# Optimization experiments

Hardware: AMD Instinct MI355X
Metric: run time of the kernel (lower is better)

## Reference

```python
import jax, jax.numpy as jnp
import numpy as np

NUM_USERS = 50000
NUM_ITEMS = 40000
EMB = 64
NNZ = 2_000_000
BATCH = 1024


def setup_inputs() -> dict:
    key = jax.random.key(0)
    ks = jax.random.split(key, 10)
    graph_rows = jax.random.randint(ks[0], (NNZ,), 0, NUM_USERS, dtype=jnp.int32)
    graph_cols = jax.random.randint(ks[1], (NNZ,), 0, NUM_ITEMS, dtype=jnp.int32)
    graph_vals = jax.random.uniform(ks[2], (NNZ,), dtype=jnp.float32)
    Wq = jax.random.normal(ks[3], (2 * EMB, NUM_ITEMS), dtype=jnp.float32) * 0.01
    bq = jnp.zeros((2 * EMB,), jnp.float32)
    Wp = jax.random.normal(ks[4], (NUM_ITEMS, EMB), dtype=jnp.float32) * 0.01
    bp = jnp.zeros((NUM_ITEMS,), jnp.float32)
    user = jax.random.randint(ks[5], (BATCH,), 0, NUM_USERS, dtype=jnp.int32)
    x = (jax.random.uniform(ks[6], (BATCH, NUM_ITEMS)) < 0.02).astype(jnp.float32)
    eps = jax.random.normal(ks[7], (NUM_USERS, EMB), dtype=jnp.float32)
    return dict(graph_vals=graph_vals, Wq=Wq, bq=bq, Wp=Wp, bp=bp, x=x,
                eps=eps, graph_rows=graph_rows, graph_cols=graph_cols, user=user)


def reference(graph_vals, Wq, bq, Wp, bp, x, eps, graph_rows, graph_cols, user):
    # ---- encode: single SpMM  h = Graph @ Wq^T + bq   (dropout off / eval mode)
    # gather item rows of Wq^T per nonzero, scale, scatter-add into users
    gathered = graph_vals[:, None] * Wq.T[graph_cols]          # [nnz, 2E]
    h = jax.ops.segment_sum(gathered, graph_rows, num_segments=NUM_USERS) + bq  # [U, 2E]
    mu, logvar = h[:, :EMB], h[:, EMB:]                        # [U, E] each
    # ---- reparameterize: z = mu + eps * exp(0.5*logvar)
    z = mu + eps * jnp.exp(0.5 * logvar)
    # ---- decode batch users: single Linear(E -> I)
    zb = z[user]                                               # [B, E]
    recon = zb @ Wp.T + bp                                     # [B, I]
    # ---- Mult-VAE ELBO (anneal = 1.0)
    log_sm = jax.nn.log_softmax(recon, axis=-1)
    recon_loss = -jnp.mean(jnp.sum(log_sm * x, axis=-1))
    mu_b, lv_b = mu[user], logvar[user]
    kl_loss = -0.5 * jnp.mean(jnp.sum(1.0 + lv_b - mu_b * mu_b - jnp.exp(lv_b), axis=-1))
    return jnp.stack([recon_loss, kl_loss])  # [2]: (recon_loss, KL_loss)
```

## Files before the change

kernel.cpp:

```cpp
#include <hip/hip_runtime.h>
#include <cstdint>

#define NUM_USERS 50000
#define NUM_ITEMS 40000
#define EMB 64
#define NNZ_E 2000000
#define BATCH 1024
#define NCHB 125
#define SLOT_CAP 128
#define INF_I 0x7fffffff
#define SC_BLK 7813

typedef __attribute__((ext_vector_type(8))) short short8;
typedef __attribute__((ext_vector_type(4))) float float4v;

__device__ __forceinline__ unsigned short f2bf(float f) {
    union { float f; unsigned u; } x; x.f = f;
    unsigned r = x.u + 0x7fffu + ((x.u >> 16) & 1u);
    return (unsigned short)(r >> 16);
}
__device__ __forceinline__ float bf2f(unsigned short s) {
    return __uint_as_float(((unsigned)s) << 16);
}
__device__ __forceinline__ unsigned pack01(float lo, float hi) {
    return __builtin_amdgcn_perm(__float_as_uint(hi), __float_as_uint(lo), 0x07060302u);
}

__global__ __launch_bounds__(256) void k_init(int* __restrict__ map, int* __restrict__ cnt,
                                              float* __restrict__ scal, int2* __restrict__ compact) {
    int t = blockIdx.x * blockDim.x + threadIdx.x;
    if (t < NUM_USERS) map[t] = INF_I;
    if (t < BATCH) cnt[t] = 0;
    if (t < 4) scal[t] = 0.f;
    if (t < BATCH * SLOT_CAP) compact[t] = make_int2(0, 0);
}

__global__ void k_map(const int* __restrict__ user, int* __restrict__ map) {
    int i = blockIdx.x * blockDim.x + threadIdx.x;
    if (i < BATCH) atomicMin(&map[user[i]], i);
}

__global__ __launch_bounds__(256) void k_prepsc(const int* __restrict__ rows,
                                                const int* __restrict__ cols,
                                                const float* __restrict__ vals,
                                                const int* __restrict__ map,
                                                int* __restrict__ cnt,
                                                int2* __restrict__ compact,
                                                const float* __restrict__ Wq,
                                                const float* __restrict__ Wp,
                                                const float* __restrict__ bp,
                                                unsigned short* __restrict__ WqT,
                                                unsigned short* __restrict__ WpBf,
                                                unsigned short* __restrict__ WpT,
                                                unsigned short* __restrict__ bpBf) {
    __shared__ float t2f[160 * 65];
    const int bid = blockIdx.x;
    const int tid = threadIdx.x;
    if (bid < SC_BLK) {
        const int e = bid * 256 + tid;
        if (e >= NNZ_E) return;
        int s = map[rows[e]];
        if (s == INF_I) return;
        int pos = atomicAdd(&cnt[s], 1);
        if (pos < SLOT_CAP) compact[s * SLOT_CAP + pos] = make_int2(cols[e], __float_as_int(vals[e]));
        return;
    }
    const int pb = bid - SC_BLK;
    if (pb < 1250) {
        const int jb = pb * 32;
        for (int idx = tid; idx < 4096; idx += 256) {
            int d = idx >> 5, c = idx & 31;
            t2f[d * 33 + c] = Wq[(size_t)d * NUM_ITEMS + jb + c];
        }
        __syncthreads();
        for (int idx = tid; idx < 4096; idx += 256) {
            int j = idx >> 7, d = idx & 127;
            WqT[(size_t)(jb + j) * 128 + d] = f2bf(t2f[d * 33 + j]);
        }
    } else if (pb < 3750) {
        const int e0 = ((pb - 1250) * 256 + tid) * 4;
        float4 w = *(const float4*)&Wp[e0];
        ushort4 o;
        o.x = f2bf(w.x); o.y = f2bf(w.y); o.z = f2bf(w.z); o.w = f2bf(w.w);
        *(ushort4*)&WpBf[e0] = o;
    } else if (pb < 4000) {
        const int j0 = (pb - 3750) * 160;
        for (int idx = tid; idx < 10240; idx += 256) {
            int jl = idx >> 6, d = idx & 63;
            t2f[jl * 65 + d] = Wp[(size_t)(j0 + jl) * 64 + d];
        }
        __syncthreads();
        for (int idx = tid; idx < 10240; idx += 256) {
            int d = idx / 160, jl = idx - d * 160;
            WpT[(size_t)d * NUM_ITEMS + j0 + jl] = f2bf(t2f[jl * 65 + d]);
        }
    } else {
        const int e0 = ((pb - 4000) * 256 + tid) * 4;
        if (e0 < NUM_ITEMS) {
            float4 w = *(const float4*)&bp[e0];
            ushort4 o;
            o.x = f2bf(w.x); o.y = f2bf(w.y); o.z = f2bf(w.z); o.w = f2bf(w.w);
            *(ushort4*)&bpBf[e0] = o;
        }
    }
}

__global__ __launch_bounds__(256) void k_hz(const int* __restrict__ user,
                                            const int* __restrict__ map,
                                            const int* __restrict__ cnt,
                                            const int2* __restrict__ compact,
                                            const unsigned short* __restrict__ WqT,
                                            const float* __restrict__ bq,
                                            const float* __restrict__ eps,
                                            unsigned short* __restrict__ zbBf,
                                            float* __restrict__ zF32,
                                            float* __restrict__ scal) {
    __shared__ float sh[4][128];
    const int i = blockIdx.x;
    const int tid = threadIdx.x;
    const int w = tid >> 6, lane = tid & 63;
    const int u = user[i];
    const int s = map[u];
    const int n8 = (min(cnt[s], SLOT_CAP) + 7) & ~7;
    const int2* cp = compact + s * SLOT_CAP;
    float ax = 0.f, ay = 0.f;
    for (int e = w; e < n8; e += 8) {
        int2 c0 = cp[e], c1 = cp[e + 4];
        ushort2 w0 = *(const ushort2*)&WqT[(size_t)c0.x * 128 + lane * 2];
        ushort2 w1 = *(const ushort2*)&WqT[(size_t)c1.x * 128 + lane * 2];
        float v0 = __int_as_float(c0.y), v1 = __int_as_float(c1.y);
        ax = fmaf(v0, bf2f(w0.x), ax);
        ay = fmaf(v0, bf2f(w0.y), ay);
        ax = fmaf(v1, bf2f(w1.x), ax);
        ay = fmaf(v1, bf2f(w1.y), ay);
    }
    sh[w][lane * 2] = ax;
    sh[w][lane * 2 + 1] = ay;
    __syncthreads();
    float h = 0.f;
    if (tid < 128) h = sh[0][tid] + sh[1][tid] + sh[2][tid] + sh[3][tid] + bq[tid];
    __syncthreads();
    if (tid < 128) sh[0][tid] = h;
    __syncthreads();
    if (tid < 64) {
        float mu = sh[0][tid];
        float lv = sh[0][tid + 64];
        float z = fmaf(eps[(size_t)u * EMB + tid], __expf(0.5f * lv), mu);
        zbBf[i * EMB + tid] = f2bf(z);
        zF32[i * EMB + tid] = z;
        float kl = 1.0f + lv - mu * mu - __expf(lv);
        #pragma unroll
        for (int o = 32; o; o >>= 1) kl += __shfl_down(kl, o);
        if (tid == 0) atomicAdd(&scal[1], kl);
    }
}

__global__ __launch_bounds__(256) void k_xz(const float* __restrict__ x,
                                            const unsigned short* __restrict__ WpT,
                                            const unsigned short* __restrict__ bpBf,
                                            const float* __restrict__ zF32,
                                            const unsigned short* __restrict__ zbBf,
                                            const unsigned short* __restrict__ WpBf,
                                            const float* __restrict__ bp,
                                            float4* __restrict__ part4) {
    const int tid = threadIdx.x;
    const int wid = tid >> 6, lane = tid & 63;
    const int l15 = lane & 15, quad = lane >> 4;
    const int kc = blockIdx.x;
    const int ibase = blockIdx.y * 128 + wid * 32;

    float4v acc[2][4], accA[2];
    #pragma unroll
    for (int mt = 0; mt < 2; mt++) {
        accA[mt] = (float4v){0.f, 0.f, 0.f, 0.f};
        #pragma unroll
        for (int nt = 0; nt < 4; nt++) acc[mt][nt] = (float4v){0.f, 0.f, 0.f, 0.f};
    }
    #pragma unroll
    for (int st = 0; st < 10; st++) {
        const int kb = kc * 320 + st * 32;
        short8 af[2];
        #pragma unroll
        for (int mt = 0; mt < 2; mt++) {
            const float* px = x + (size_t)(ibase + mt * 16 + l15) * NUM_ITEMS + kb + quad * 8;
            float4 a0 = *(const float4*)px;
            float4 a1 = *(const float4*)(px + 4);
            union { short8 s; unsigned u[4]; } v;
            v.u[0] = pack01(a0.x, a0.y);
            v.u[1] = pack01(a0.z, a0.w);
            v.u[2] = pack01(a1.x, a1.y);
            v.u[3] = pack01(a1.z, a1.w);
            af[mt] = v.s;
        }
        short8 bfr[4];
        #pragma unroll
        for (int nt = 0; nt < 4; nt++)
            bfr[nt] = *(const short8*)&WpT[(size_t)(nt * 16 + l15) * NUM_ITEMS + kb + quad * 8];
        short8 ab;
        if (l15 == 0) {
            ab = *(const short8*)&bpBf[kb + quad * 8];
        } else if (l15 == 1) {
            short o = (short)0x3F80;
            ab = (short8){o, o, o, o, o, o, o, o};
        } else {
            ab = (short8){0, 0, 0, 0, 0, 0, 0, 0};
        }
        #pragma unroll
        for (int mt = 0; mt < 2; mt++) {
            #pragma unroll
            for (int nt = 0; nt < 4; nt++)
                acc[mt][nt] = __builtin_amdgcn_mfma_f32_16x16x32_bf16(
                    af[mt], bfr[nt], acc[mt][nt], 0, 0, 0);
            accA[mt] = __builtin_amdgcn_mfma_f32_16x16x32_bf16(
                    af[mt], ab, accA[mt], 0, 0, 0);
        }
    }
    float c_s[2][4], sx_s[2][4];
    #pragma unroll
    for (int mt = 0; mt < 2; mt++) {
        #pragma unroll
        for (int r = 0; r < 4; r++) {
            const int row = ibase + mt * 16 + quad * 4 + r;
            float dxp = 0.f;
            #pragma unroll
            for (int nt = 0; nt < 4; nt++)
                dxp += zF32[(size_t)row * EMB + nt * 16 + l15] * acc[mt][nt][r];
            #pragma unroll
            for (int d = 1; d < 16; d <<= 1) dxp += __shfl_xor(dxp, d);
            sx_s[mt][r] = __shfl(accA[mt][r], (lane & 48) + 1);
            c_s[mt][r] = dxp + accA[mt][r];
        }
    }

    short8 zf[2][2];
    #pragma unroll
    for (int mt = 0; mt < 2; mt++) {
        const unsigned short* pa = zbBf + (size_t)(ibase + mt * 16 + l15) * EMB + quad * 8;
        zf[mt][0] = *(const short8*)pa;
        zf[mt][1] = *(const short8*)(pa + 32);
    }
    float m_run[2][4], s_run[2][4];
    #pragma unroll
    for (int mt = 0; mt < 2; mt++)
        #pragma unroll
        for (int r = 0; r < 4; r++) { m_run[mt][r] = -1e30f; s_run[mt][r] = 0.f; }

    #pragma unroll
    for (int c5 = 0; c5 < 5; c5++) {
        const int jb = kc * 320 + c5 * 64;
        short8 bfr2[4][2];
        #pragma unroll
        for (int nt = 0; nt < 4; nt++) {
            const unsigned short* pb = WpBf + (size_t)(jb + nt * 16 + l15) * EMB + quad * 8;
            bfr2[nt][0] = *(const short8*)pb;
            bfr2[nt][1] = *(const short8*)(pb + 32);
        }
        float4v accz[2][4];
        #pragma unroll
        for (int mt = 0; mt < 2; mt++)
            #pragma unroll
            for (int nt = 0; nt < 4; nt++)
                accz[mt][nt] = (float4v){0.f, 0.f, 0.f, 0.f};
        #pragma unroll
        for (int kh = 0; kh < 2; kh++)
            #pragma unroll
            for (int mt = 0; mt < 2; mt++)
                #pragma unroll
                for (int nt = 0; nt < 4; nt++)
                    accz[mt][nt] = __builtin_amdgcn_mfma_f32_16x16x32_bf16(
                        zf[mt][kh], bfr2[nt][kh], accz[mt][nt], 0, 0, 0);
        float bpv[4];
        #pragma unroll
        for (int nt = 0; nt < 4; nt++) bpv[nt] = bp[jb + nt * 16 + l15];
        #pragma unroll
        for (int mt = 0; mt < 2; mt++) {
            #pragma unroll
            for (int r = 0; r < 4; r++) {
                float v0 = accz[mt][0][r] + bpv[0];
                float v1 = accz[mt][1][r] + bpv[1];
                float v2 = accz[mt][2][r] + bpv[2];
                float v3 = accz[mt][3][r] + bpv[3];
                float mx = fmaxf(fmaxf(v0, v1), fmaxf(v2, v3));
                float M2 = fmaxf(m_run[mt][r], mx);
                float ls = __expf(v0 - M2) + __expf(v1 - M2) +
                           __expf(v2 - M2) + __expf(v3 - M2);
                s_run[mt][r] = s_run[mt][r] * __expf(m_run[mt][r] - M2) + ls;
                m_run[mt][r] = M2;
            }
        }
    }
    #pragma unroll
    for (int d = 1; d < 16; d <<= 1) {
        #pragma unroll
        for (int mt = 0; mt < 2; mt++)
            #pragma unroll
            for (int r = 0; r < 4; r++) {
                float m2 = __shfl_xor(m_run[mt][r], d);
                float s2 = __shfl_xor(s_run[mt][r], d);
                float M = fmaxf(m_run[mt][r], m2);
                s_run[mt][r] = s_run[mt][r] * __expf(m_run[mt][r] - M)
                             + s2 * __expf(m2 - M);
                m_run[mt][r] = M;
            }
    }
    if (l15 == 0) {
        #pragma unroll
        for (int mt = 0; mt < 2; mt++)
            #pragma unroll
            for (int r = 0; r < 4; r++) {
                const int row = ibase + mt * 16 + quad * 4 + r;
                part4[(size_t)row * NCHB + kc] =
                    make_float4(m_run[mt][r], s_run[mt][r], c_s[mt][r], sx_s[mt][r]);
            }
    }
}

__global__ __launch_bounds__(64) void k_merge(const float4* __restrict__ part4,
                                              float* __restrict__ scal,
                                              float* __restrict__ out) {
    const int row = blockIdx.x;
    const int lane = threadIdx.x;
    float M = -1e30f, S = 0.f, dxc = 0.f, sx = 0.f;
    for (int c = lane; c < NCHB; c += 64) {
        float4 p = part4[(size_t)row * NCHB + c];
        float M2 = fmaxf(M, p.x);
        S = S * __expf(M - M2) + p.y * __expf(p.x - M2);
        M = M2; dxc += p.z; sx += p.w;
    }
    #pragma unroll
    for (int o = 1; o < 64; o <<= 1) {
        float M2 = __shfl_xor(M, o);
        float S2 = __shfl_xor(S, o);
        float Mn = fmaxf(M, M2);
        S = S * __expf(M - Mn) + S2 * __expf(M2 - Mn);
        M = Mn;
        dxc += __shfl_xor(dxc, o);
        sx += __shfl_xor(sx, o);
    }
    if (lane == 0) {
        float lse = M + logf(S);
        atomicAdd(&scal[0], dxc - lse * sx);
        __threadfence();
        unsigned done = atomicAdd((unsigned*)&scal[2], 1u);
        if (done == BATCH - 1) {
            float recon = atomicAdd(&scal[0], 0.f);
            float kl = atomicAdd(&scal[1], 0.f);
            out[0] = -recon * (1.0f / BATCH);
            out[1] = -0.5f * kl * (1.0f / BATCH);
        }
    }
}

extern "C" void kernel_launch(void* const* d_in, const int* in_sizes, int n_in,
                              void* d_out, int out_size, void* d_ws, size_t ws_size,
                              hipStream_t stream) {
    const float* graph_vals = (const float*)d_in[0];
    const float* Wq         = (const float*)d_in[1];
    const float* bq         = (const float*)d_in[2];
    const float* Wp         = (const float*)d_in[3];
    const float* bp         = (const float*)d_in[4];
    const float* x          = (const float*)d_in[5];
    const float* eps        = (const float*)d_in[6];
    const int*   graph_rows = (const int*)d_in[7];
    const int*   graph_cols = (const int*)d_in[8];
    const int*   user       = (const int*)d_in[9];
    float* out = (float*)d_out;

    char* ws = (char*)d_ws;
    int*            map     = (int*)(ws + 0);
    int*            cnt     = (int*)(ws + 200704);
    float*          scal    = (float*)(ws + 204800);
    int2*           compact = (int2*)(ws + 205056);
    unsigned short* zbBf    = (unsigned short*)(ws + 1253632);
    float*          zF32    = (float*)(ws + 1384704);
    float4*         part4   = (float4*)(ws + 1646848);
    unsigned short* WpBf    = (unsigned short*)(ws + 3694848);
    unsigned short* WqT     = (unsigned short*)(ws + 8814848);
    unsigned short* WpT     = (unsigned short*)(ws + 19054848);
    unsigned short* bpBf    = (unsigned short*)(ws + 24174848);

    k_init<<<512, 256, 0, stream>>>(map, cnt, scal, compact);
    k_map<<<4, 256, 0, stream>>>(user, map);
    k_prepsc<<<SC_BLK + 4040, 256, 0, stream>>>(graph_rows, graph_cols, graph_vals, map, cnt,
                                                compact, Wq, Wp, bp, WqT, WpBf, WpT, bpBf);
    k_hz<<<BATCH, 256, 0, stream>>>(user, map, cnt, compact, WqT, bq, eps, zbBf, zF32, scal);
    dim3 g(NCHB, BATCH / 128);
    k_xz<<<g, 256, 0, stream>>>(x, WpT, bpBf, zF32, zbBf, WpBf, bp, part4);
    k_merge<<<BATCH, 64, 0, stream>>>(part4, scal, out);
}
```

Before: 388.9 us.

## Split scatter and weight prep kernels; use one-wave blocks for xz

```diff
diff --git a/kernel.cpp b/kernel.cpp
--- a/kernel.cpp
+++ b/kernel.cpp
@@ -9,7 +9,6 @@
 #define NCHB 125
 #define SLOT_CAP 128
 #define INF_I 0x7fffffff
-#define SC_BLK 7813
 
 typedef __attribute__((ext_vector_type(8))) short short8;
 typedef __attribute__((ext_vector_type(4))) float float4v;
@@ -40,34 +39,32 @@
     if (i < BATCH) atomicMin(&map[user[i]], i);
 }
 
-__global__ __launch_bounds__(256) void k_prepsc(const int* __restrict__ rows,
-                                                const int* __restrict__ cols,
-                                                const float* __restrict__ vals,
-                                                const int* __restrict__ map,
-                                                int* __restrict__ cnt,
-                                                int2* __restrict__ compact,
-                                                const float* __restrict__ Wq,
-                                                const float* __restrict__ Wp,
-                                                const float* __restrict__ bp,
-                                                unsigned short* __restrict__ WqT,
-                                                unsigned short* __restrict__ WpBf,
-                                                unsigned short* __restrict__ WpT,
-                                                unsigned short* __restrict__ bpBf) {
-    __shared__ float t2f[160 * 65];
+__global__ __launch_bounds__(256) void k_scatter(const int* __restrict__ rows,
+                                                 const int* __restrict__ cols,
+                                                 const float* __restrict__ vals,
+                                                 const int* __restrict__ map,
+                                                 int* __restrict__ cnt,
+                                                 int2* __restrict__ compact) {
+    const int e = blockIdx.x * 256 + threadIdx.x;
+    if (e >= NNZ_E) return;
+    int s = map[rows[e]];
+    if (s == INF_I) return;
+    int pos = atomicAdd(&cnt[s], 1);
+    if (pos < SLOT_CAP) compact[s * SLOT_CAP + pos] = make_int2(cols[e], __float_as_int(vals[e]));
+}
+
+__global__ __launch_bounds__(256) void k_prep(const float* __restrict__ Wq,
+                                              const float* __restrict__ Wp,
+                                              const float* __restrict__ bp,
+                                              unsigned short* __restrict__ WqT,
+                                              unsigned short* __restrict__ WpBf,
+                                              unsigned short* __restrict__ WpT,
+                                              unsigned short* __restrict__ bpBf) {
+    __shared__ float t2f[4224];
     const int bid = blockIdx.x;
     const int tid = threadIdx.x;
-    if (bid < SC_BLK) {
-        const int e = bid * 256 + tid;
-        if (e >= NNZ_E) return;
-        int s = map[rows[e]];
-        if (s == INF_I) return;
-        int pos = atomicAdd(&cnt[s], 1);
-        if (pos < SLOT_CAP) compact[s * SLOT_CAP + pos] = make_int2(cols[e], __float_as_int(vals[e]));
-        return;
-    }
-    const int pb = bid - SC_BLK;
-    if (pb < 1250) {
-        const int jb = pb * 32;
+    if (bid < 1250) {
+        const int jb = bid * 32;
         for (int idx = tid; idx < 4096; idx += 256) {
             int d = idx >> 5, c = idx & 31;
             t2f[d * 33 + c] = Wq[(size_t)d * NUM_ITEMS + jb + c];
@@ -77,25 +74,25 @@
             int j = idx >> 7, d = idx & 127;
             WqT[(size_t)(jb + j) * 128 + d] = f2bf(t2f[d * 33 + j]);
         }
-    } else if (pb < 3750) {
-        const int e0 = ((pb - 1250) * 256 + tid) * 4;
+    } else if (bid < 3750) {
+        const int e0 = ((bid - 1250) * 256 + tid) * 4;
         float4 w = *(const float4*)&Wp[e0];
         ushort4 o;
         o.x = f2bf(w.x); o.y = f2bf(w.y); o.z = f2bf(w.z); o.w = f2bf(w.w);
         *(ushort4*)&WpBf[e0] = o;
-    } else if (pb < 4000) {
-        const int j0 = (pb - 3750) * 160;
-        for (int idx = tid; idx < 10240; idx += 256) {
+    } else if (bid < 4375) {
+        const int j0 = (bid - 3750) * 64;
+        for (int idx = tid; idx < 4096; idx += 256) {
             int jl = idx >> 6, d = idx & 63;
             t2f[jl * 65 + d] = Wp[(size_t)(j0 + jl) * 64 + d];
         }
         __syncthreads();
-        for (int idx = tid; idx < 10240; idx += 256) {
-            int d = idx / 160, jl = idx - d * 160;
+        for (int idx = tid; idx < 4096; idx += 256) {
+            int d = idx >> 6, jl = idx & 63;
             WpT[(size_t)d * NUM_ITEMS + j0 + jl] = f2bf(t2f[jl * 65 + d]);
         }
     } else {
-        const int e0 = ((pb - 4000) * 256 + tid) * 4;
+        const int e0 = ((bid - 4375) * 256 + tid) * 4;
         if (e0 < NUM_ITEMS) {
             float4 w = *(const float4*)&bp[e0];
             ushort4 o;
@@ -155,19 +152,18 @@
     }
 }
 
-__global__ __launch_bounds__(256) void k_xz(const float* __restrict__ x,
-                                            const unsigned short* __restrict__ WpT,
-                                            const unsigned short* __restrict__ bpBf,
-                                            const float* __restrict__ zF32,
-                                            const unsigned short* __restrict__ zbBf,
-                                            const unsigned short* __restrict__ WpBf,
-                                            const float* __restrict__ bp,
-                                            float4* __restrict__ part4) {
-    const int tid = threadIdx.x;
-    const int wid = tid >> 6, lane = tid & 63;
+__global__ __launch_bounds__(64) void k_xz(const float* __restrict__ x,
+                                           const unsigned short* __restrict__ WpT,
+                                           const unsigned short* __restrict__ bpBf,
+                                           const float* __restrict__ zF32,
+                                           const unsigned short* __restrict__ zbBf,
+                                           const unsigned short* __restrict__ WpBf,
+                                           const float* __restrict__ bp,
+                                           float4* __restrict__ part4) {
+    const int lane = threadIdx.x;
     const int l15 = lane & 15, quad = lane >> 4;
     const int kc = blockIdx.x;
-    const int ibase = blockIdx.y * 128 + wid * 32;
+    const int ibase = blockIdx.y * 32;
 
     float4v acc[2][4], accA[2];
     #pragma unroll
@@ -381,10 +377,10 @@
 
     k_init<<<512, 256, 0, stream>>>(map, cnt, scal, compact);
     k_map<<<4, 256, 0, stream>>>(user, map);
-    k_prepsc<<<SC_BLK + 4040, 256, 0, stream>>>(graph_rows, graph_cols, graph_vals, map, cnt,
-                                                compact, Wq, Wp, bp, WqT, WpBf, WpT, bpBf);
+    k_scatter<<<7813, 256, 0, stream>>>(graph_rows, graph_cols, graph_vals, map, cnt, compact);
+    k_prep<<<4415, 256, 0, stream>>>(Wq, Wp, bp, WqT, WpBf, WpT, bpBf);
     k_hz<<<BATCH, 256, 0, stream>>>(user, map, cnt, compact, WqT, bq, eps, zbBf, zF32, scal);
-    dim3 g(NCHB, BATCH / 128);
-    k_xz<<<g, 256, 0, stream>>>(x, WpT, bpBf, zF32, zbBf, WpBf, bp, part4);
+    dim3 g(NCHB, 32);
+    k_xz<<<g, 64, 0, stream>>>(x, WpT, bpBf, zF32, zbBf, WpBf, bp, part4);
     k_merge<<<BATCH, 64, 0, stream>>>(part4, scal, out);
 }
```

Result: no change. 390.6 us (+0.4%).

## Stage Wp tiles in LDS and software-pipeline x loads in k_xz

Applied to the files above, without the earlier changes.

```diff
diff --git a/kernel.cpp b/kernel.cpp
--- a/kernel.cpp
+++ b/kernel.cpp
@@ -53,7 +53,7 @@
                                                 unsigned short* __restrict__ WpBf,
                                                 unsigned short* __restrict__ WpT,
                                                 unsigned short* __restrict__ bpBf) {
-    __shared__ float t2f[160 * 65];
+    __shared__ float t2f[4224];
     const int bid = blockIdx.x;
     const int tid = threadIdx.x;
     if (bid < SC_BLK) {
@@ -83,19 +83,19 @@
         ushort4 o;
         o.x = f2bf(w.x); o.y = f2bf(w.y); o.z = f2bf(w.z); o.w = f2bf(w.w);
         *(ushort4*)&WpBf[e0] = o;
-    } else if (pb < 4000) {
-        const int j0 = (pb - 3750) * 160;
-        for (int idx = tid; idx < 10240; idx += 256) {
+    } else if (pb < 4375) {
+        const int j0 = (pb - 3750) * 64;
+        for (int idx = tid; idx < 4096; idx += 256) {
             int jl = idx >> 6, d = idx & 63;
             t2f[jl * 65 + d] = Wp[(size_t)(j0 + jl) * 64 + d];
         }
         __syncthreads();
-        for (int idx = tid; idx < 10240; idx += 256) {
-            int d = idx / 160, jl = idx - d * 160;
+        for (int idx = tid; idx < 4096; idx += 256) {
+            int d = idx >> 6, jl = idx & 63;
             WpT[(size_t)d * NUM_ITEMS + j0 + jl] = f2bf(t2f[jl * 65 + d]);
         }
     } else {
-        const int e0 = ((pb - 4000) * 256 + tid) * 4;
+        const int e0 = ((pb - 4375) * 256 + tid) * 4;
         if (e0 < NUM_ITEMS) {
             float4 w = *(const float4*)&bp[e0];
             ushort4 o;
@@ -163,12 +163,24 @@
                                             const unsigned short* __restrict__ WpBf,
                                             const float* __restrict__ bp,
                                             float4* __restrict__ part4) {
+    __shared__ unsigned short wlds[23040];
+    __shared__ unsigned short bpblds[320];
+    __shared__ float bplds[320];
     const int tid = threadIdx.x;
     const int wid = tid >> 6, lane = tid & 63;
     const int l15 = lane & 15, quad = lane >> 4;
     const int kc = blockIdx.x;
     const int ibase = blockIdx.y * 128 + wid * 32;
 
+    for (int c = tid; c < 2560; c += 256) {
+        int row = c / 40, off = c % 40;
+        short8 v = *(const short8*)&WpT[(size_t)row * NUM_ITEMS + kc * 320 + off * 8];
+        *(short8*)&wlds[row * 328 + off * 8] = v;
+    }
+    if (tid < 40)
+        *(short8*)&bpblds[tid * 8] = *(const short8*)&bpBf[kc * 320 + tid * 8];
+    __syncthreads();
+
     float4v acc[2][4], accA[2];
     #pragma unroll
     for (int mt = 0; mt < 2; mt++) {
@@ -176,35 +188,48 @@
         #pragma unroll
         for (int nt = 0; nt < 4; nt++) acc[mt][nt] = (float4v){0.f, 0.f, 0.f, 0.f};
     }
+    float4 xr[2][2][2];
+    #pragma unroll
+    for (int mt = 0; mt < 2; mt++) {
+        const float* px = x + (size_t)(ibase + mt * 16 + l15) * NUM_ITEMS + kc * 320 + quad * 8;
+        xr[0][mt][0] = *(const float4*)px;
+        xr[0][mt][1] = *(const float4*)(px + 4);
+    }
     #pragma unroll
     for (int st = 0; st < 10; st++) {
-        const int kb = kc * 320 + st * 32;
-        short8 af[2];
-        #pragma unroll
-        for (int mt = 0; mt < 2; mt++) {
-            const float* px = x + (size_t)(ibase + mt * 16 + l15) * NUM_ITEMS + kb + quad * 8;
-            float4 a0 = *(const float4*)px;
-            float4 a1 = *(const float4*)(px + 4);
-            union { short8 s; unsigned u[4]; } v;
-            v.u[0] = pack01(a0.x, a0.y);
-            v.u[1] = pack01(a0.z, a0.w);
-            v.u[2] = pack01(a1.x, a1.y);
-            v.u[3] = pack01(a1.z, a1.w);
-            af[mt] = v.s;
+        const int cur = st & 1, nxt = cur ^ 1;
+        if (st < 9) {
+            #pragma unroll
+            for (int mt = 0; mt < 2; mt++) {
+                const float* px = x + (size_t)(ibase + mt * 16 + l15) * NUM_ITEMS
+                                    + kc * 320 + (st + 1) * 32 + quad * 8;
+                xr[nxt][mt][0] = *(const float4*)px;
+                xr[nxt][mt][1] = *(const float4*)(px + 4);
+            }
         }
         short8 bfr[4];
         #pragma unroll
         for (int nt = 0; nt < 4; nt++)
-            bfr[nt] = *(const short8*)&WpT[(size_t)(nt * 16 + l15) * NUM_ITEMS + kb + quad * 8];
+            bfr[nt] = *(const short8*)&wlds[(nt * 16 + l15) * 328 + st * 32 + quad * 8];
         short8 ab;
         if (l15 == 0) {
-            ab = *(const short8*)&bpBf[kb + quad * 8];
+            ab = *(const short8*)&bpblds[st * 32 + quad * 8];
         } else if (l15 == 1) {
             short o = (short)0x3F80;
             ab = (short8){o, o, o, o, o, o, o, o};
         } else {
             ab = (short8){0, 0, 0, 0, 0, 0, 0, 0};
         }
+        short8 af[2];
+        #pragma unroll
+        for (int mt = 0; mt < 2; mt++) {
+            union { short8 s; unsigned u[4]; } v;
+            v.u[0] = pack01(xr[cur][mt][0].x, xr[cur][mt][0].y);
+            v.u[1] = pack01(xr[cur][mt][0].z, xr[cur][mt][0].w);
+            v.u[2] = pack01(xr[cur][mt][1].x, xr[cur][mt][1].y);
+            v.u[3] = pack01(xr[cur][mt][1].z, xr[cur][mt][1].w);
+            af[mt] = v.s;
+        }
         #pragma unroll
         for (int mt = 0; mt < 2; mt++) {
             #pragma unroll
@@ -232,6 +257,15 @@
         }
     }
 
+    __syncthreads();
+    for (int c = tid; c < 2560; c += 256) {
+        int row = c >> 3, off = c & 7;
+        short8 v = *(const short8*)&WpBf[(size_t)(kc * 320 + row) * 64 + off * 8];
+        *(short8*)&wlds[row * 72 + off * 8] = v;
+    }
+    if (tid < 320) bplds[tid] = bp[kc * 320 + tid];
+    __syncthreads();
+
     short8 zf[2][2];
     #pragma unroll
     for (int mt = 0; mt < 2; mt++) {
@@ -247,13 +281,13 @@
 
     #pragma unroll
     for (int c5 = 0; c5 < 5; c5++) {
-        const int jb = kc * 320 + c5 * 64;
         short8 bfr2[4][2];
         #pragma unroll
         for (int nt = 0; nt < 4; nt++) {
-            const unsigned short* pb = WpBf + (size_t)(jb + nt * 16 + l15) * EMB + quad * 8;
-            bfr2[nt][0] = *(const short8*)pb;
-            bfr2[nt][1] = *(const short8*)(pb + 32);
+            #pragma unroll
+            for (int kh = 0; kh < 2; kh++)
+                bfr2[nt][kh] = *(const short8*)&wlds[(c5 * 64 + nt * 16 + l15) * 72
+                                                     + kh * 32 + quad * 8];
         }
         float4v accz[2][4];
         #pragma unroll
@@ -271,7 +305,7 @@
                         zf[mt][kh], bfr2[nt][kh], accz[mt][nt], 0, 0, 0);
         float bpv[4];
         #pragma unroll
-        for (int nt = 0; nt < 4; nt++) bpv[nt] = bp[jb + nt * 16 + l15];
+        for (int nt = 0; nt < 4; nt++) bpv[nt] = bplds[c5 * 64 + nt * 16 + l15];
         #pragma unroll
         for (int mt = 0; mt < 2; mt++) {
             #pragma unroll
@@ -381,10 +415,10 @@
 
     k_init<<<512, 256, 0, stream>>>(map, cnt, scal, compact);
     k_map<<<4, 256, 0, stream>>>(user, map);
-    k_prepsc<<<SC_BLK + 4040, 256, 0, stream>>>(graph_rows, graph_cols, graph_vals, map, cnt,
+    k_prepsc<<<SC_BLK + 4415, 256, 0, stream>>>(graph_rows, graph_cols, graph_vals, map, cnt,
                                                 compact, Wq, Wp, bp, WqT, WpBf, WpT, bpBf);
     k_hz<<<BATCH, 256, 0, stream>>>(user, map, cnt, compact, WqT, bq, eps, zbBf, zF32, scal);
-    dim3 g(NCHB, BATCH / 128);
+    dim3 g(NCHB, 8);
     k_xz<<<g, 256, 0, stream>>>(x, WpT, bpBf, zF32, zbBf, WpBf, bp, part4);
     k_merge<<<BATCH, 64, 0, stream>>>(part4, scal, out);
 }
```

After: 378.8 us. 2.6% less time.
